# Optimization experiments

Hardware: AMD Instinct MI355X
Metric: run time of the kernel (lower is better)

## Reference

```python
import jax, jax.numpy as jnp
import numpy as np

B, S, H = 32, 512, 256
MAX_MEL = 2000  # init kwarg max_mel_len
DUR_MAX = 8


def setup_inputs() -> dict:
    key = jax.random.key(0)
    k1, k2 = jax.random.split(key)
    x = jax.random.normal(k1, (B, S, H), dtype=jnp.float32)
    duration = jax.random.randint(k2, (B, S), 0, DUR_MAX, dtype=jnp.int32)
    return {"x": x, "duration": duration, "max_len": MAX_MEL}


def reference(x, duration, max_len):
    # x: [B, S, H]; duration: [B, S] int; max_len unused (kept for API parity).
    batch, seq_len, hidden = x.shape
    max_mel = MAX_MEL

    cumsum = jnp.cumsum(duration, axis=1)            # [B, S]
    pos = jnp.arange(max_mel, dtype=cumsum.dtype)    # [T]

    # Original builds mask = (pos < cumsum[:, :, None]) and takes argmax over S
    # (index of first True), falling back to seq_len-1 when no True, then clamps.
    # That is exactly searchsorted(cumsum, pos, side='right') clipped to S-1:
    # first j with cumsum[j] > pos; returns S (-> clipped to S-1) when pos >= total.
    idx = jax.vmap(lambda c: jnp.searchsorted(c, pos, side='right'))(cumsum)  # [B, T]
    idx = jnp.clip(idx, 0, seq_len - 1)

    output = jnp.take_along_axis(x, idx[:, :, None], axis=1)  # [B, T, H]

    mel_len = jnp.clip(jnp.sum(duration, axis=1), None, max_mel).astype(jnp.int32)  # [B]
    return output, mel_len
```

## Files before the change

### kernel.cpp

```cpp
#include <hip/hip_runtime.h>

constexpr int B_ = 32;
constexpr int S_ = 512;
constexpr int H_ = 256;
constexpr int T_ = 2000;
constexpr int F4 = H_ / 4;
constexpr int ROWS_PER_BLOCK = 32;
constexpr int NBLK_T = (T_ + ROWS_PER_BLOCK - 1) / ROWS_PER_BLOCK;

typedef float f32x4 __attribute__((ext_vector_type(4)));

__global__ __launch_bounds__(256) void lenreg_fused_kernel(
    const f32x4* __restrict__ x,
    const int* __restrict__ dur,
    const int* __restrict__ max_len_p,
    f32x4* __restrict__ out,
    float* __restrict__ mel_len_out)
{
    const int b = blockIdx.y;
    const int tid = threadIdx.x;
    const int lane = tid & 63;
    const int wave = tid >> 6;

    __shared__ int s_cum[S_];
    __shared__ int s_wsum[4];

    const int2 d2 = ((const int2*)(dur + b * S_))[tid];
    const int pair = d2.x + d2.y;
    int scan = pair;
#pragma unroll
    for (int off = 1; off < 64; off <<= 1) {
        const int y = __shfl_up(scan, off);
        if (lane >= off) scan += y;
    }
    if (lane == 63) s_wsum[wave] = scan;
    __syncthreads();
    int wprefix = 0;
#pragma unroll
    for (int w = 0; w < 4; ++w) wprefix += (w < wave) ? s_wsum[w] : 0;
    const int excl = wprefix + scan - pair;
    s_cum[2 * tid]     = excl + d2.x;
    s_cum[2 * tid + 1] = excl + pair;
    __syncthreads();

    if (blockIdx.x == 0 && tid == 0) {
        const int total = s_cum[S_ - 1];
        const int ml = max_len_p[0];
        mel_len_out[b] = (float)(total < ml ? total : ml);
    }

    const f32x4* __restrict__ x_b = x + (size_t)b * S_ * F4;
    f32x4* __restrict__ out_b = out + (size_t)b * T_ * F4;

    const int t0 = blockIdx.x * ROWS_PER_BLOCK;
#pragma unroll
    for (int i = 0; i < ROWS_PER_BLOCK / 4; ++i) {
        const int t = t0 + i * 4 + wave;
        if (t < T_) {
            int lo = 0, hi = S_;
#pragma unroll
            for (int step = 0; step < 9; ++step) {
                const int mid = (lo + hi) >> 1;
                if (s_cum[mid] <= t) lo = mid + 1; else hi = mid;
            }
            const int idx = lo < (S_ - 1) ? lo : (S_ - 1);
            const f32x4 v = x_b[(size_t)idx * F4 + lane];
            __builtin_nontemporal_store(v, &out_b[(size_t)t * F4 + lane]);
        }
    }
}

extern "C" void kernel_launch(void* const* d_in, const int* in_sizes, int n_in,
                              void* d_out, int out_size, void* d_ws, size_t ws_size,
                              hipStream_t stream) {
    const f32x4* x = (const f32x4*)d_in[0];
    const int* duration = (const int*)d_in[1];
    const int* max_len_p = (const int*)d_in[2];

    float* out = (float*)d_out;
    float* mel_len_out = out + (size_t)B_ * T_ * H_;

    dim3 grid(NBLK_T, B_);
    lenreg_fused_kernel<<<grid, 256, 0, stream>>>(
        x, duration, max_len_p, (f32x4*)out, mel_len_out);
}
```

Baseline: 87.96 us.

## Replace per-output binary search gather with per-source scatter plus tail fill

Instead of each output frame doing a binary search over the cumulative durations and gathering an input row, each block now owns 16 source rows and writes each row into its contiguous output span (cumsum[s-1]..cumsum[s]). Separate tail blocks fill frames past the total length with the last row and write mel_len. This removes the binary search and redundant reads of x. In exchange, work per wave varies with the durations, and the serial per-row store loops may balance poorly.

```diff
diff --git a/kernel.cpp b/kernel.cpp
--- a/kernel.cpp
+++ b/kernel.cpp
@@ -5,12 +5,14 @@
 constexpr int H_ = 256;
 constexpr int T_ = 2000;
 constexpr int F4 = H_ / 4;
-constexpr int ROWS_PER_BLOCK = 32;
-constexpr int NBLK_T = (T_ + ROWS_PER_BLOCK - 1) / ROWS_PER_BLOCK;
+constexpr int RPS = 16;
+constexpr int N_SCAT = S_ / RPS;
+constexpr int TAIL_CHUNK = 125;
+constexpr int N_TAIL = (T_ + TAIL_CHUNK - 1) / TAIL_CHUNK;
 
 typedef float f32x4 __attribute__((ext_vector_type(4)));
 
-__global__ __launch_bounds__(256) void lenreg_fused_kernel(
+__global__ __launch_bounds__(256) void lenreg_scatter_kernel(
     const f32x4* __restrict__ x,
     const int* __restrict__ dur,
     const int* __restrict__ max_len_p,
@@ -18,6 +20,7 @@
     float* __restrict__ mel_len_out)
 {
     const int b = blockIdx.y;
+    const int role = blockIdx.x;
     const int tid = threadIdx.x;
     const int lane = tid & 63;
     const int wave = tid >> 6;
@@ -43,29 +46,37 @@
     s_cum[2 * tid + 1] = excl + pair;
     __syncthreads();
 
-    if (blockIdx.x == 0 && tid == 0) {
-        const int total = s_cum[S_ - 1];
-        const int ml = max_len_p[0];
-        mel_len_out[b] = (float)(total < ml ? total : ml);
-    }
-
+    const int total = s_cum[S_ - 1];
     const f32x4* __restrict__ x_b = x + (size_t)b * S_ * F4;
     f32x4* __restrict__ out_b = out + (size_t)b * T_ * F4;
 
-    const int t0 = blockIdx.x * ROWS_PER_BLOCK;
+    if (role < N_SCAT) {
+        const int s0 = role * RPS + wave * (RPS / 4);
+        f32x4 v[RPS / 4];
 #pragma unroll
-    for (int i = 0; i < ROWS_PER_BLOCK / 4; ++i) {
-        const int t = t0 + i * 4 + wave;
-        if (t < T_) {
-            int lo = 0, hi = S_;
+        for (int i = 0; i < RPS / 4; ++i)
+            v[i] = x_b[(size_t)(s0 + i) * F4 + lane];
 #pragma unroll
-            for (int step = 0; step < 9; ++step) {
-                const int mid = (lo + hi) >> 1;
-                if (s_cum[mid] <= t) lo = mid + 1; else hi = mid;
-            }
-            const int idx = lo < (S_ - 1) ? lo : (S_ - 1);
-            const f32x4 v = x_b[(size_t)idx * F4 + lane];
-            __builtin_nontemporal_store(v, &out_b[(size_t)t * F4 + lane]);
+        for (int i = 0; i < RPS / 4; ++i) {
+            const int s = s0 + i;
+            const int lo = s ? s_cum[s - 1] : 0;
+            int hi = s_cum[s]; if (hi > T_) hi = T_;
+            for (int t = lo; t < hi; ++t)
+                __builtin_nontemporal_store(v[i], &out_b[(size_t)t * F4 + lane]);
+        }
+    } else {
+        const int j = role - N_SCAT;
+        if (j == 0 && tid == 0) {
+            const int ml = max_len_p[0];
+            mel_len_out[b] = (float)(total < ml ? total : ml);
+        }
+        int t_begin = j * TAIL_CHUNK;
+        int t_end = t_begin + TAIL_CHUNK; if (t_end > T_) t_end = T_;
+        if (t_begin < total) t_begin = total;
+        if (t_begin < t_end) {
+            const f32x4 v = x_b[(size_t)(S_ - 1) * F4 + lane];
+            for (int t = t_begin + wave; t < t_end; t += 4)
+                __builtin_nontemporal_store(v, &out_b[(size_t)t * F4 + lane]);
         }
     }
 }
@@ -80,7 +91,7 @@
     float* out = (float*)d_out;
     float* mel_len_out = out + (size_t)B_ * T_ * H_;
 
-    dim3 grid(NBLK_T, B_);
-    lenreg_fused_kernel<<<grid, 256, 0, stream>>>(
+    dim3 grid(N_SCAT + N_TAIL, B_);
+    lenreg_scatter_kernel<<<grid, 256, 0, stream>>>(
         x, duration, max_len_p, (f32x4*)out, mel_len_out);
 }
```

Result: no change. 89.28 us (+1.5%).
